# Kernel tuning notes

Hardware: AMD Instinct MI355X
Metric: run time of the kernel (lower is better)

Reference implementation:

```python
import jax, jax.numpy as jnp
import numpy as np
from jax import lax

GAMMA = 0.1  # fixed RBF bandwidth from LearnableRBFInfluence


def setup_inputs() -> dict:
    key = jax.random.key(0)
    k1, k2, k3, k4 = jax.random.split(key, 4)
    B, H, W = 2, 256, 256
    NUM_FILTERS, KS, NUM_BASIS = 48, 7, 31
    u_log = jax.random.normal(k1, (B, 1, H, W), jnp.float32)
    f_log = jax.random.normal(k2, (B, 1, H, W), jnp.float32)
    filters = jax.random.normal(k3, (NUM_FILTERS, 1, KS, KS), jnp.float32) * 0.05
    rbf_weights = jax.random.normal(k4, (NUM_FILTERS, NUM_BASIS), jnp.float32) * 0.05
    lambda_param = jnp.float32(0.1)
    return {"u_log": u_log, "f_log": f_log, "filters": filters,
            "rbf_weights": rbf_weights, "lambda_param": lambda_param}


def reference(u_log, f_log, filters, rbf_weights, lambda_param):
    # Batched form of the per-filter loop:
    #   conv[i] = conv2d(u, k_i)  ->  one grouped conv with 48 output channels
    num_basis = rbf_weights.shape[1]
    mu = jnp.linspace(-1.0, 1.0, num_basis).astype(u_log.dtype)  # [K]

    dn = lax.conv_dimension_numbers(u_log.shape, filters.shape, ('NCHW', 'OIHW', 'NCHW'))
    conv = lax.conv_general_dilated(u_log, filters, (1, 1), 'SAME',
                                    dimension_numbers=dn)  # [B,48,H,W]

    # RBF influence, per filter channel c: phi = sum_k w[c,k] * exp(-(conv-mu_k)^2/(2 g^2))
    diff = conv[..., None] - mu                              # [B,48,H,W,K]
    rbf = jnp.exp(-(diff * diff) / (2.0 * GAMMA * GAMMA))
    phi = jnp.einsum('bchwk,ck->bchw', rbf, rbf_weights)     # [B,48,H,W]

    # Per-filter conv2d(phi_i, flip(k_i)) summed over i == single conv
    # with OIHW weight [1,48,7,7] built from spatially-flipped filters.
    kT = jnp.flip(filters, axis=(2, 3)).transpose(1, 0, 2, 3)  # [1,48,7,7]
    dn2 = lax.conv_dimension_numbers(phi.shape, kT.shape, ('NCHW', 'OIHW', 'NCHW'))
    diffusion = lax.conv_general_dilated(phi, kT, (1, 1), 'SAME',
                                         dimension_numbers=dn2)  # [B,1,H,W]

    reaction = lambda_param * (u_log - f_log)
    return u_log - diffusion - reaction
```

## Files before the change

kernel.cpp:

```cpp
#include <hip/hip_runtime.h>

#define HH 256
#define WW 256
#define NPIX (2 * HH * WW)
#define NC 48
#define NB 31
#define TP 192

#define OTY 32
#define OTX 64
#define PTY 38
#define PSTR2 76
#define N1ITEM 684

#define PADW 272
#define PADN (2 * PADW * PADW)

#define PW1N (24 * 49)
#define PW2N (48 * 8 * 7)

#define OT 32
#define PT 38
#define PSTR 44
#define UT 44
#define USTR 52


typedef float f32x2 __attribute__((ext_vector_type(2)));

__device__ __forceinline__ f32x2 splat2(float v) {
    f32x2 r; r.x = v; r.y = v; return r;
}
__device__ __forceinline__ f32x2 pkfma(f32x2 a, f32x2 b, f32x2 c) {
    return __builtin_elementwise_fma(a, b, c);
}

__global__ __launch_bounds__(256)
void tnrd_prep(const float* __restrict__ wr,
               const float* __restrict__ u,
               const float* __restrict__ wf,
               float2* __restrict__ tab,
               float* __restrict__ upad,
               float2* __restrict__ pw1,
               float2* __restrict__ pw2)
{
    const int bid = blockIdx.x;
    const int tid = threadIdx.x;
    {
        const int i = bid * 256 + tid;
        const int img = i / (PADW * PADW);
        const int rem = i - img * (PADW * PADW);
        const int py = rem / PADW, px = rem - py * PADW;
        const int gy = py - 6, gx = px - 6;
        float v = 0.f;
        if ((unsigned)gy < HH && (unsigned)gx < WW)
            v = u[img * (HH * WW) + gy * WW + gx];
        upad[i] = v;
    }
    if (bid < NC && tid < TP) {
        const int j = tid;
        const float* rc = wr + bid * NB;
        float v0 = 0.f, v1 = 0.f;
        float x0 = fmaf((float)j, 1.0f / 64.0f, -1.5f);
        float x1 = x0 + 1.0f / 64.0f;
        #pragma unroll
        for (int k = 0; k < NB; ++k) {
            float mu = -1.f + (float)k * (1.f / 15.f);
            float d0 = x0 - mu, d1 = x1 - mu;
            float w = rc[k];
            v0 = fmaf(w, __expf(-50.f * d0 * d0), v0);
            v1 = fmaf(w, __expf(-50.f * d1 * d1), v1);
        }
        tab[bid * TP + j] = make_float2(v0, v1 - v0);
    }
    if (bid == 48) {
        for (int i = tid; i < PW1N; i += 256) {
            int pr = i / 49, k = i - pr * 49;
            pw1[i] = make_float2(wf[(2 * pr) * 49 + k],
                                 wf[(2 * pr + 1) * 49 + k]);
        }
    }
    if (bid == 49) {
        for (int i = tid; i < PW2N; i += 256) {
            int c = i / 56, r = i - c * 56;
            int dyt = r / 7, wi = r - dyt * 7;
            float lo = (dyt < 7) ? wf[c * 49 + (6 - dyt) * 7 + wi] : 0.f;
            float hi = (dyt > 0) ? wf[c * 49 + (7 - dyt) * 7 + wi] : 0.f;
            pw2[i] = make_float2(lo, hi);
        }
    }
}

__global__ __launch_bounds__(256)
void tnrd_table(const float* __restrict__ wr, float2* __restrict__ tab)
{
    const int ch = blockIdx.x;
    const float* rc = wr + ch * NB;
    for (int j = threadIdx.x; j < TP; j += 256) {
        float v0 = 0.f, v1 = 0.f;
        float x0 = fmaf((float)j, 1.0f / 64.0f, -1.5f);
        float x1 = x0 + 1.0f / 64.0f;
        #pragma unroll
        for (int k = 0; k < NB; ++k) {
            float mu = -1.f + (float)k * (1.f / 15.f);
            float d0 = x0 - mu, d1 = x1 - mu;
            float w = rc[k];
            v0 = fmaf(w, __expf(-50.f * d0 * d0), v0);
            v1 = fmaf(w, __expf(-50.f * d1 * d1), v1);
        }
        tab[ch * TP + j] = make_float2(v0, v1 - v0);
    }
}

#define F1STEPP(WI, s0, s1, s2, s3)                                     \
    { f32x2 w_ = wp[WI];                                                \
      ab0 = pkfma(splat2(s0), w_, ab0);                                 \
      ab1 = pkfma(splat2(s1), w_, ab1);                                 \
      ab2 = pkfma(splat2(s2), w_, ab2);                                 \
      ab3 = pkfma(splat2(s3), w_, ab3); }

#define F1ROWP(WPROW, q0, q1, q2)                                       \
    { const f32x2* wp = (WPROW);                                        \
      F1STEPP(0, q0.x, q0.y, q0.z, q0.w)                                \
      F1STEPP(1, q0.y, q0.z, q0.w, q1.x)                                \
      F1STEPP(2, q0.z, q0.w, q1.x, q1.y)                                \
      F1STEPP(3, q0.w, q1.x, q1.y, q1.z)                                \
      F1STEPP(4, q1.x, q1.y, q1.z, q1.w)                                \
      F1STEPP(5, q1.y, q1.z, q1.w, q2.x)                                \
      F1STEPP(6, q1.z, q1.w, q2.x, q2.y) }

#define LERP1(res, aval, T)                                             \
    { float t_ = fminf(fmaxf(fmaf(aval, 64.f, 96.f), 0.f), 191.999f);   \
      float fj_ = floorf(t_);                                           \
      float2 e_ = (T)[(int)fj_];               \
      res = fmaf(t_ - fj_, e_.y, e_.x); }

#define C2STEPP(WI, s0, s1, s2, s3, t0, t1, t2, t3)                     \
    { f32x2 wa_ = wpa[WI], wb_ = wpb[WI];                               \
      oo0 = pkfma(splat2(s0), wa_, oo0);                                \
      oo1 = pkfma(splat2(s1), wa_, oo1);                                \
      oo2 = pkfma(splat2(s2), wa_, oo2);                                \
      oo3 = pkfma(splat2(s3), wa_, oo3);                                \
      oo0 = pkfma(splat2(t0), wb_, oo0);                                \
      oo1 = pkfma(splat2(t1), wb_, oo1);                                \
      oo2 = pkfma(splat2(t2), wb_, oo2);                                \
      oo3 = pkfma(splat2(t3), wb_, oo3); }

#define C2SWEEPP()                                                      \
    C2STEPP(6, A0.x, A0.y, A0.z, A0.w, B0.x, B0.y, B0.z, B0.w)          \
    C2STEPP(5, A0.y, A0.z, A0.w, A1.x, B0.y, B0.z, B0.w, B1.x)          \
    C2STEPP(4, A0.z, A0.w, A1.x, A1.y, B0.z, B0.w, B1.x, B1.y)          \
    C2STEPP(3, A0.w, A1.x, A1.y, A1.z, B0.w, B1.x, B1.y, B1.z)          \
    C2STEPP(2, A1.x, A1.y, A1.z, A1.w, B1.x, B1.y, B1.z, B1.w)          \
    C2STEPP(1, A1.y, A1.z, A1.w, A2.x, B1.y, B1.z, B1.w, B2.x)          \
    C2STEPP(0, A1.z, A1.w, A2.x, A2.y, B1.z, B1.w, B2.x, B2.y)

__global__ __launch_bounds__(256, 6)
void tnrd_main_pk(const float* __restrict__ upad,
                  const f32x2* __restrict__ pw1,
                  const f32x2* __restrict__ pw2,
                  const float2* __restrict__ tab,
                  float* __restrict__ part)
{
    __shared__ __align__(16) float phi_s[2][PTY * PSTR2];

    const int tid = threadIdx.x;
    const int bx = blockIdx.x, by = blockIdx.y;
    const int b = blockIdx.z / 24, g = blockIdx.z % 24;
    const int c0 = g * 2;

    const int py0 = by * OTY - 3, px0 = bx * OTX - 3;

    {
        const f32x2* wpb0 = pw1 + g * 49;
        const float2* tA = tab + c0 * TP;
        const float2* tB = tA + TP;
        const float* ubase = upad + b * (PADW * PADW);
        for (int p = 0; p < 3; ++p) {
            const int gi = tid + p * 256;
            if (gi < N1ITEM) {
                const int pr = gi / 18, pc = (gi % 18) * 4;
                f32x2 ab0 = {0.f, 0.f}, ab1 = {0.f, 0.f};
                f32x2 ab2 = {0.f, 0.f}, ab3 = {0.f, 0.f};
                const float* bptr = ubase + (py0 + pr + 3) * PADW
                                          + (bx * OTX + pc);

                float4 c0v = *(const float4*)(bptr);
                float4 c1v = *(const float4*)(bptr + 4);
                float2 c2v = *(const float2*)(bptr + 8);
                #pragma unroll 1
                for (int dy = 0; dy < 6; ++dy) {
                    const float* nr = bptr + (dy + 1) * PADW;
                    float4 n0 = *(const float4*)(nr);
                    float4 n1 = *(const float4*)(nr + 4);
                    float2 n2 = *(const float2*)(nr + 8);
                    F1ROWP(wpb0 + dy * 7, c0v, c1v, c2v)
                    c0v = n0; c1v = n1; c2v = n2;
                }
                F1ROWP(wpb0 + 42, c0v, c1v, c2v)

                const int gy = py0 + pr;
                const bool rowok = (unsigned)gy < HH;
                const bool ok0 = rowok && (unsigned)(px0 + pc + 0) < WW;
                const bool ok1 = rowok && (unsigned)(px0 + pc + 1) < WW;
                const bool ok2 = rowok && (unsigned)(px0 + pc + 2) < WW;
                const bool ok3 = rowok && (unsigned)(px0 + pc + 3) < WW;
                float pA0, pA1, pA2, pA3, pB0, pB1, pB2, pB3;
                LERP1(pA0, ab0.x, tA) LERP1(pB0, ab0.y, tB)
                LERP1(pA1, ab1.x, tA) LERP1(pB1, ab1.y, tB)
                LERP1(pA2, ab2.x, tA) LERP1(pB2, ab2.y, tB)
                LERP1(pA3, ab3.x, tA) LERP1(pB3, ab3.y, tB)
                pA0 = ok0 ? pA0 : 0.f;  pB0 = ok0 ? pB0 : 0.f;
                pA1 = ok1 ? pA1 : 0.f;  pB1 = ok1 ? pB1 : 0.f;
                pA2 = ok2 ? pA2 : 0.f;  pB2 = ok2 ? pB2 : 0.f;
                pA3 = ok3 ? pA3 : 0.f;  pB3 = ok3 ? pB3 : 0.f;
                *(float4*)(&phi_s[0][pr * PSTR2 + pc]) =
                    make_float4(pA0, pA1, pA2, pA3);
                *(float4*)(&phi_s[1][pr * PSTR2 + pc]) =
                    make_float4(pB0, pB1, pB2, pB3);
            }
        }
    }
    __syncthreads();

    {
        const int tr = tid >> 4;
        const int ox = (tid & 15) * 4;
        f32x2 oo0 = {0.f, 0.f}, oo1 = {0.f, 0.f};
        f32x2 oo2 = {0.f, 0.f}, oo3 = {0.f, 0.f};

        #pragma unroll
        for (int dyt = 0; dyt < 8; ++dyt) {
            const float* rA = &phi_s[0][(2 * tr + dyt) * PSTR2 + ox];
            const float* rB = &phi_s[1][(2 * tr + dyt) * PSTR2 + ox];
            const float4 A0 = *(const float4*)(rA);
            const float4 A1 = *(const float4*)(rA + 4);
            const float2 A2 = *(const float2*)(rA + 8);
            const float4 B0 = *(const float4*)(rB);
            const float4 B1 = *(const float4*)(rB + 4);
            const float2 B2 = *(const float2*)(rB + 8);
            const f32x2* wpa = pw2 + (size_t)c0 * 56 + dyt * 7;
            const f32x2* wpb = wpa + 56;
            C2SWEEPP()
        }

        const int gy0 = by * OTY + 2 * tr, gx = bx * OTX + ox;
        float* dst = part + (size_t)g * NPIX + b * (HH * WW) + gy0 * WW + gx;
        *reinterpret_cast<float4*>(dst) =
            make_float4(oo0.x, oo1.x, oo2.x, oo3.x);
        *reinterpret_cast<float4*>(dst + WW) =
            make_float4(oo0.y, oo1.y, oo2.y, oo3.y);
    }
}

#define F1STEP(WI, s0, s1, s2, s3)                                      \
    { float fa = wa[WI], fb = wb[WI];                                   \
      a0 = fmaf(s0, fa, a0); a1 = fmaf(s1, fa, a1);                     \
      a2 = fmaf(s2, fa, a2); a3 = fmaf(s3, fa, a3);                     \
      b0 = fmaf(s0, fb, b0); b1 = fmaf(s1, fb, b1);                     \
      b2 = fmaf(s2, fb, b2); b3 = fmaf(s3, fb, b3); }

#define F1ROW(WA, WB, q0, q1, q2)                                       \
    { const float* wa = (WA); const float* wb = (WB);                   \
      F1STEP(0, q0.x, q0.y, q0.z, q0.w)                                 \
      F1STEP(1, q0.y, q0.z, q0.w, q1.x)                                 \
      F1STEP(2, q0.z, q0.w, q1.x, q1.y)                                 \
      F1STEP(3, q0.w, q1.x, q1.y, q1.z)                                 \
      F1STEP(4, q1.x, q1.y, q1.z, q1.w)                                 \
      F1STEP(5, q1.y, q1.z, q1.w, q2.x)                                 \
      F1STEP(6, q1.z, q1.w, q2.x, q2.y) }

#define C2STEP(WI, s0, s1, s2, s3, t0, t1, t2, t3)                      \
    { float fa = wra[WI], fb = wrb[WI];                                 \
      o0 = fmaf(s0, fa, o0); o1 = fmaf(s1, fa, o1);                     \
      o2 = fmaf(s2, fa, o2); o3 = fmaf(s3, fa, o3);                     \
      o0 = fmaf(t0, fb, o0); o1 = fmaf(t1, fb, o1);                     \
      o2 = fmaf(t2, fb, o2); o3 = fmaf(t3, fb, o3); }

template<int CPG>
__global__ __launch_bounds__(256, 6)
void tnrd_main(const float* __restrict__ u,
               const float* __restrict__ wf,
               const float2* __restrict__ tab,
               float* __restrict__ part)
{
    constexpr int NGRP = NC / CPG;
    constexpr int NPASS = CPG / 2;
    __shared__ __align__(16) float u_s[UT * USTR];
    __shared__ __align__(16) float phi_s[2][PT * PSTR];

    const int tid = threadIdx.x;
    const int bx = blockIdx.x, by = blockIdx.y;
    const int b = blockIdx.z / NGRP, g = blockIdx.z % NGRP;
    const int c0g = g * CPG;

    const int uy0 = by * OT - 6, ux0 = bx * OT - 6;
    const float* ub = u + b * (HH * WW);
    for (int i = tid; i < UT * USTR; i += 256) {
        int r = i / USTR, c = i - r * USTR;
        int gy = uy0 + r, gx = ux0 + c;
        float v = 0.f;
        if (c < UT && (unsigned)gy < HH && (unsigned)gx < WW)
            v = ub[gy * WW + gx];
        u_s[i] = v;
    }
    __syncthreads();

    const int oy = tid >> 3;
    const int ox0 = (tid & 7) * 4;
    float o0 = 0.f, o1 = 0.f, o2 = 0.f, o3 = 0.f;
    const int py0 = by * OT - 3, px0 = bx * OT - 3;

    auto conv1_pass = [&](int cp, float* __restrict__ bufA,
                          float* __restrict__ bufB) {
        const float* wA = wf + (c0g + 2 * cp) * 49;
        const float* wB = wA + 49;
        const float2* tA = tab + (c0g + 2 * cp) * TP;
        const float2* tB = tA + TP;
        for (int p = 0; p < 2; ++p) {
            const int gi = tid + p * 256;
            if (gi < PT * 10) {
                const int pr = gi % PT, pc = (gi / PT) * 4;
                float a0 = 0.f, a1 = 0.f, a2 = 0.f, a3 = 0.f;
                float b0 = 0.f, b1 = 0.f, b2 = 0.f, b3 = 0.f;
                const float* bptr = &u_s[pr * USTR + pc];
                float4 c0 = *(const float4*)(bptr);
                float4 c1 = *(const float4*)(bptr + 4);
                float2 c2 = *(const float2*)(bptr + 8);
                #pragma unroll 1
                for (int dy = 0; dy < 6; ++dy) {
                    const float* nr = bptr + (dy + 1) * USTR;
                    float4 n0 = *(const float4*)(nr);
                    float4 n1 = *(const float4*)(nr + 4);
                    float2 n2 = *(const float2*)(nr + 8);
                    F1ROW(wA + dy * 7, wB + dy * 7, c0, c1, c2)
                    c0 = n0; c1 = n1; c2 = n2;
                }
                F1ROW(wA + 42, wB + 42, c0, c1, c2)
                const int gy = py0 + pr;
                const bool rowok = (unsigned)gy < HH;
                const bool ok0 = rowok && (unsigned)(px0 + pc + 0) < WW;
                const bool ok1 = rowok && (unsigned)(px0 + pc + 1) < WW;
                const bool ok2 = rowok && (unsigned)(px0 + pc + 2) < WW;
                const bool ok3 = rowok && (unsigned)(px0 + pc + 3) < WW;
                float pA0, pA1, pA2, pA3, pB0, pB1, pB2, pB3;
                LERP1(pA0, a0, tA) LERP1(pB0, b0, tB)
                LERP1(pA1, a1, tA) LERP1(pB1, b1, tB)
                LERP1(pA2, a2, tA) LERP1(pB2, b2, tB)
                LERP1(pA3, a3, tA) LERP1(pB3, b3, tB)
                pA0 = ok0 ? pA0 : 0.f;  pB0 = ok0 ? pB0 : 0.f;
                pA1 = ok1 ? pA1 : 0.f;  pB1 = ok1 ? pB1 : 0.f;
                pA2 = ok2 ? pA2 : 0.f;  pB2 = ok2 ? pB2 : 0.f;
                pA3 = ok3 ? pA3 : 0.f;  pB3 = ok3 ? pB3 : 0.f;
                *(float4*)(bufA + pr * PSTR + pc) =
                    make_float4(pA0, pA1, pA2, pA3);
                *(float4*)(bufB + pr * PSTR + pc) =
                    make_float4(pB0, pB1, pB2, pB3);
            }
        }
    };

    #pragma unroll 1
    for (int pass = 0; pass < NPASS; ++pass) {
        conv1_pass(pass, phi_s[0], phi_s[1]);
        __syncthreads();
        const float* wA = wf + (c0g + 2 * pass) * 49;
        const float* wB = wA + 49;
        const float* pA = phi_s[0];
        const float* pB = phi_s[1];
        for (int dy = 0; dy < 7; ++dy) {
            const float* rA = pA + (oy + dy) * PSTR + ox0;
            const float* rB = pB + (oy + dy) * PSTR + ox0;
            const float4 A0 = *(const float4*)(rA);
            const float4 A1 = *(const float4*)(rA + 4);
            const float2 A2 = *(const float2*)(rA + 8);
            const float4 B0 = *(const float4*)(rB);
            const float4 B1 = *(const float4*)(rB + 4);
            const float2 B2 = *(const float2*)(rB + 8);
            const float* wra = wA + (6 - dy) * 7;
            const float* wrb = wB + (6 - dy) * 7;
            C2STEP(6, A0.x, A0.y, A0.z, A0.w, B0.x, B0.y, B0.z, B0.w)
            C2STEP(5, A0.y, A0.z, A0.w, A1.x, B0.y, B0.z, B0.w, B1.x)
            C2STEP(4, A0.z, A0.w, A1.x, A1.y, B0.z, B0.w, B1.x, B1.y)
            C2STEP(3, A0.w, A1.x, A1.y, A1.z, B0.w, B1.x, B1.y, B1.z)
            C2STEP(2, A1.x, A1.y, A1.z, A1.w, B1.x, B1.y, B1.z, B1.w)
            C2STEP(1, A1.y, A1.z, A1.w, A2.x, B1.y, B1.z, B1.w, B2.x)
            C2STEP(0, A1.z, A1.w, A2.x, A2.y, B1.z, B1.w, B2.x, B2.y)
        }
        if (pass < NPASS - 1) __syncthreads();
    }

    const int gy = by * OT + oy, gx = bx * OT + ox0;
    float4 v4 = make_float4(o0, o1, o2, o3);
    *reinterpret_cast<float4*>(part + (size_t)g * NPIX + b * (HH * WW)
                               + gy * WW + gx) = v4;
}

template<int NGRP>
__global__ __launch_bounds__(256)
void combine_kernel(const float* __restrict__ u,
                    const float* __restrict__ f,
                    const float* __restrict__ lam,
                    const float* __restrict__ part,
                    float* __restrict__ out)
{
    int i = blockIdx.x * 256 + threadIdx.x;
    float d = 0.f;
    #pragma unroll
    for (int g = 0; g < NGRP; ++g) d += part[g * NPIX + i];
    float lv = lam[0];
    float uv = u[i];
    float fv = f[i];
    out[i] = uv - d - lv * (uv - fv);
}

extern "C" void kernel_launch(void* const* d_in, const int* in_sizes, int n_in,
                              void* d_out, int out_size, void* d_ws, size_t ws_size,
                              hipStream_t stream) {
    const float* u    = (const float*)d_in[0];
    const float* f    = (const float*)d_in[1];
    const float* filt = (const float*)d_in[2];
    const float* rbfw = (const float*)d_in[3];
    const float* lam  = (const float*)d_in[4];
    float* out = (float*)d_out;
    float* part = (float*)d_ws;
    float2* tabg = (float2*)d_out;

    float* upad = part + (size_t)24 * NPIX;
    float* pw1f = upad + PADN;
    float* pw2f = pw1f + 2 * PW1N;
    const size_t need =
        ((size_t)24 * NPIX + PADN + 2 * PW1N + 2 * PW2N) * sizeof(float);
    if (ws_size >= need) {
        tnrd_prep<<<PADN / 256, 256, 0, stream>>>(
            rbfw, u, filt, tabg, upad, (float2*)pw1f, (float2*)pw2f);
        tnrd_main_pk<<<dim3(WW / OTX, HH / OTY, 48), 256, 0, stream>>>(
            upad, (const f32x2*)pw1f, (const f32x2*)pw2f, tabg, part);
        combine_kernel<24><<<512, 256, 0, stream>>>(u, f, lam, part, out);
    } else if (ws_size >= (size_t)12 * NPIX * sizeof(float)) {
        tnrd_table<<<NC, 256, 0, stream>>>(rbfw, tabg);
        tnrd_main<4><<<dim3(8, 8, 24), 256, 0, stream>>>(u, filt, tabg, part);
        combine_kernel<12><<<512, 256, 0, stream>>>(u, f, lam, part, out);
    } else {
        tnrd_table<<<NC, 256, 0, stream>>>(rbfw, tabg);
        tnrd_main<8><<<dim3(8, 8, 12), 256, 0, stream>>>(u, filt, tabg, part);
        combine_kernel<6><<<512, 256, 0, stream>>>(u, f, lam, part, out);
    }
}
```

Baseline: 95.83 us.

## Stage RBF tables in LDS and software-pipeline both conv stages

Each block now copies its two channels' RBF lookup tables into shared memory, so the per-pixel table gathers hit LDS instead of global memory. The first conv stage is unrolled into explicit work items whose table gathers are issued before earlier items are finished, letting gather latency overlap the next item's FMA work. The second conv stage double-buffers its LDS row loads so the next row is fetched while the current one is being used. In exchange the kernel needs more registers and an extra barrier, which may lower occupancy under the 6-blocks-per-SM launch bound.

```diff
diff --git a/kernel.cpp b/kernel.cpp
--- a/kernel.cpp
+++ b/kernel.cpp
@@ -129,11 +129,68 @@
       F1STEPP(5, q1.y, q1.z, q1.w, q2.x)                                \
       F1STEPP(6, q1.z, q1.w, q2.x, q2.y) }
 
-#define LERP1(res, aval, T)                                             \
+#define GISS(fr, e, aval, T)                                            \
     { float t_ = fminf(fmaxf(fmaf(aval, 64.f, 96.f), 0.f), 191.999f);   \
       float fj_ = floorf(t_);                                           \
-      float2 e_ = (T)[(int)fj_];               \
-      res = fmaf(t_ - fj_, e_.y, e_.x); }
+      fr = t_ - fj_;                                                    \
+      e = (T)[(int)fj_]; }
+
+#define C1_CONV(S, GI)                                                  \
+    const int pr##S = (GI) / 18, pc##S = ((GI) % 18) * 4;               \
+    f32x2 aba##S = {0.f, 0.f}, abb##S = {0.f, 0.f},                     \
+          abc##S = {0.f, 0.f}, abd##S = {0.f, 0.f};                     \
+    {                                                                   \
+        f32x2 &ab0 = aba##S, &ab1 = abb##S, &ab2 = abc##S, &ab3 = abd##S;\
+        const float* bptr = ubase + (py0 + pr##S + 3) * PADW            \
+                                  + (bx * OTX + pc##S);                 \
+        float4 c0v = *(const float4*)(bptr);                            \
+        float4 c1v = *(const float4*)(bptr + 4);                        \
+        float2 c2v = *(const float2*)(bptr + 8);                        \
+        _Pragma("unroll 1")                                             \
+        for (int dy = 0; dy < 6; ++dy) {                                \
+            const float* nr = bptr + (dy + 1) * PADW;                   \
+            float4 n0 = *(const float4*)(nr);                           \
+            float4 n1 = *(const float4*)(nr + 4);                       \
+            float2 n2 = *(const float2*)(nr + 8);                       \
+            F1ROWP(wpb0 + dy * 7, c0v, c1v, c2v)                        \
+            c0v = n0; c1v = n1; c2v = n2;                               \
+        }                                                               \
+        F1ROWP(wpb0 + 42, c0v, c1v, c2v)                                \
+    }
+
+#define C1_GATHER(S)                                                    \
+    float fA0##S, fA1##S, fA2##S, fA3##S, fB0##S, fB1##S, fB2##S, fB3##S;\
+    float2 eA0##S, eA1##S, eA2##S, eA3##S, eB0##S, eB1##S, eB2##S, eB3##S;\
+    GISS(fA0##S, eA0##S, aba##S.x, tAl) GISS(fB0##S, eB0##S, aba##S.y, tBl)\
+    GISS(fA1##S, eA1##S, abb##S.x, tAl) GISS(fB1##S, eB1##S, abb##S.y, tBl)\
+    GISS(fA2##S, eA2##S, abc##S.x, tAl) GISS(fB2##S, eB2##S, abc##S.y, tBl)\
+    GISS(fA3##S, eA3##S, abd##S.x, tAl) GISS(fB3##S, eB3##S, abd##S.y, tBl)
+
+#define C1_FIN(S)                                                       \
+    {                                                                   \
+        const int gy = py0 + pr##S;                                     \
+        const bool rowok = (unsigned)gy < HH;                           \
+        const bool ok0 = rowok && (unsigned)(px0 + pc##S + 0) < WW;     \
+        const bool ok1 = rowok && (unsigned)(px0 + pc##S + 1) < WW;     \
+        const bool ok2 = rowok && (unsigned)(px0 + pc##S + 2) < WW;     \
+        const bool ok3 = rowok && (unsigned)(px0 + pc##S + 3) < WW;     \
+        float pA0 = fmaf(fA0##S, eA0##S.y, eA0##S.x);                   \
+        float pB0 = fmaf(fB0##S, eB0##S.y, eB0##S.x);                   \
+        float pA1 = fmaf(fA1##S, eA1##S.y, eA1##S.x);                   \
+        float pB1 = fmaf(fB1##S, eB1##S.y, eB1##S.x);                   \
+        float pA2 = fmaf(fA2##S, eA2##S.y, eA2##S.x);                   \
+        float pB2 = fmaf(fB2##S, eB2##S.y, eB2##S.x);                   \
+        float pA3 = fmaf(fA3##S, eA3##S.y, eA3##S.x);                   \
+        float pB3 = fmaf(fB3##S, eB3##S.y, eB3##S.x);                   \
+        pA0 = ok0 ? pA0 : 0.f;  pB0 = ok0 ? pB0 : 0.f;                  \
+        pA1 = ok1 ? pA1 : 0.f;  pB1 = ok1 ? pB1 : 0.f;                  \
+        pA2 = ok2 ? pA2 : 0.f;  pB2 = ok2 ? pB2 : 0.f;                  \
+        pA3 = ok3 ? pA3 : 0.f;  pB3 = ok3 ? pB3 : 0.f;                  \
+        *(float4*)(&phi_s[0][pr##S * PSTR2 + pc##S]) =                  \
+            make_float4(pA0, pA1, pA2, pA3);                            \
+        *(float4*)(&phi_s[1][pr##S * PSTR2 + pc##S]) =                  \
+            make_float4(pB0, pB1, pB2, pB3);                            \
+    }
 
 #define C2STEPP(WI, s0, s1, s2, s3, t0, t1, t2, t3)                     \
     { f32x2 wa_ = wpa[WI], wb_ = wpb[WI];                               \
@@ -156,69 +213,43 @@
     C2STEPP(0, A1.z, A1.w, A2.x, A2.y, B1.z, B1.w, B2.x, B2.y)
 
 __global__ __launch_bounds__(256, 6)
-void tnrd_main_pk(const float* __restrict__ upad,
+void tnrd_main_pl(const float* __restrict__ upad,
                   const f32x2* __restrict__ pw1,
                   const f32x2* __restrict__ pw2,
                   const float2* __restrict__ tab,
                   float* __restrict__ part)
 {
     __shared__ __align__(16) float phi_s[2][PTY * PSTR2];
+    __shared__ __align__(16) float2 tabs[2][TP];
 
     const int tid = threadIdx.x;
     const int bx = blockIdx.x, by = blockIdx.y;
     const int b = blockIdx.z / 24, g = blockIdx.z % 24;
     const int c0 = g * 2;
 
+    for (int i = tid; i < 2 * TP; i += 256)
+        ((float2*)tabs)[i] = tab[c0 * TP + i];
+    __syncthreads();
+
     const int py0 = by * OTY - 3, px0 = bx * OTX - 3;
+    const f32x2* wpb0 = pw1 + g * 49;
+    const float2* tAl = tabs[0];
+    const float2* tBl = tabs[1];
+    const float* ubase = upad + b * (PADW * PADW);
 
     {
-        const f32x2* wpb0 = pw1 + g * 49;
-        const float2* tA = tab + c0 * TP;
-        const float2* tB = tA + TP;
-        const float* ubase = upad + b * (PADW * PADW);
-        for (int p = 0; p < 3; ++p) {
-            const int gi = tid + p * 256;
-            if (gi < N1ITEM) {
-                const int pr = gi / 18, pc = (gi % 18) * 4;
-                f32x2 ab0 = {0.f, 0.f}, ab1 = {0.f, 0.f};
-                f32x2 ab2 = {0.f, 0.f}, ab3 = {0.f, 0.f};
-                const float* bptr = ubase + (py0 + pr + 3) * PADW
-                                          + (bx * OTX + pc);
-
-                float4 c0v = *(const float4*)(bptr);
-                float4 c1v = *(const float4*)(bptr + 4);
-                float2 c2v = *(const float2*)(bptr + 8);
-                #pragma unroll 1
-                for (int dy = 0; dy < 6; ++dy) {
-                    const float* nr = bptr + (dy + 1) * PADW;
-                    float4 n0 = *(const float4*)(nr);
-                    float4 n1 = *(const float4*)(nr + 4);
-                    float2 n2 = *(const float2*)(nr + 8);
-                    F1ROWP(wpb0 + dy * 7, c0v, c1v, c2v)
-                    c0v = n0; c1v = n1; c2v = n2;
-                }
-                F1ROWP(wpb0 + 42, c0v, c1v, c2v)
-
-                const int gy = py0 + pr;
-                const bool rowok = (unsigned)gy < HH;
-                const bool ok0 = rowok && (unsigned)(px0 + pc + 0) < WW;
-                const bool ok1 = rowok && (unsigned)(px0 + pc + 1) < WW;
-                const bool ok2 = rowok && (unsigned)(px0 + pc + 2) < WW;
-                const bool ok3 = rowok && (unsigned)(px0 + pc + 3) < WW;
-                float pA0, pA1, pA2, pA3, pB0, pB1, pB2, pB3;
-                LERP1(pA0, ab0.x, tA) LERP1(pB0, ab0.y, tB)
-                LERP1(pA1, ab1.x, tA) LERP1(pB1, ab1.y, tB)
-                LERP1(pA2, ab2.x, tA) LERP1(pB2, ab2.y, tB)
-                LERP1(pA3, ab3.x, tA) LERP1(pB3, ab3.y, tB)
-                pA0 = ok0 ? pA0 : 0.f;  pB0 = ok0 ? pB0 : 0.f;
-                pA1 = ok1 ? pA1 : 0.f;  pB1 = ok1 ? pB1 : 0.f;
-                pA2 = ok2 ? pA2 : 0.f;  pB2 = ok2 ? pB2 : 0.f;
-                pA3 = ok3 ? pA3 : 0.f;  pB3 = ok3 ? pB3 : 0.f;
-                *(float4*)(&phi_s[0][pr * PSTR2 + pc]) =
-                    make_float4(pA0, pA1, pA2, pA3);
-                *(float4*)(&phi_s[1][pr * PSTR2 + pc]) =
-                    make_float4(pB0, pB1, pB2, pB3);
-            }
+        C1_CONV(X, tid)
+        C1_GATHER(X)
+        C1_CONV(Y, tid + 256)
+        C1_GATHER(Y)
+        C1_FIN(X)
+        if (tid < N1ITEM - 512) {
+            C1_CONV(Z, tid + 512)
+            C1_GATHER(Z)
+            C1_FIN(Y)
+            C1_FIN(Z)
+        } else {
+            C1_FIN(Y)
         }
     }
     __syncthreads();
@@ -229,19 +260,39 @@
         f32x2 oo0 = {0.f, 0.f}, oo1 = {0.f, 0.f};
         f32x2 oo2 = {0.f, 0.f}, oo3 = {0.f, 0.f};
 
+        const float* rA0 = &phi_s[0][(2 * tr) * PSTR2 + ox];
+        const float* rB0 = &phi_s[1][(2 * tr) * PSTR2 + ox];
+        float4 A0c = *(const float4*)(rA0);
+        float4 A1c = *(const float4*)(rA0 + 4);
+        float2 A2c = *(const float2*)(rA0 + 8);
+        float4 B0c = *(const float4*)(rB0);
+        float4 B1c = *(const float4*)(rB0 + 4);
+        float2 B2c = *(const float2*)(rB0 + 8);
+
         #pragma unroll
         for (int dyt = 0; dyt < 8; ++dyt) {
-            const float* rA = &phi_s[0][(2 * tr + dyt) * PSTR2 + ox];
-            const float* rB = &phi_s[1][(2 * tr + dyt) * PSTR2 + ox];
-            const float4 A0 = *(const float4*)(rA);
-            const float4 A1 = *(const float4*)(rA + 4);
-            const float2 A2 = *(const float2*)(rA + 8);
-            const float4 B0 = *(const float4*)(rB);
-            const float4 B1 = *(const float4*)(rB + 4);
-            const float2 B2 = *(const float2*)(rB + 8);
-            const f32x2* wpa = pw2 + (size_t)c0 * 56 + dyt * 7;
-            const f32x2* wpb = wpa + 56;
-            C2SWEEPP()
+            float4 A0n, A1n, B0n, B1n; float2 A2n, B2n;
+            if (dyt < 7) {
+                const float* nA = &phi_s[0][(2 * tr + dyt + 1) * PSTR2 + ox];
+                const float* nB = &phi_s[1][(2 * tr + dyt + 1) * PSTR2 + ox];
+                A0n = *(const float4*)(nA);
+                A1n = *(const float4*)(nA + 4);
+                A2n = *(const float2*)(nA + 8);
+                B0n = *(const float4*)(nB);
+                B1n = *(const float4*)(nB + 4);
+                B2n = *(const float2*)(nB + 8);
+            }
+            {
+                const float4 A0 = A0c, A1 = A1c; const float2 A2 = A2c;
+                const float4 B0 = B0c, B1 = B1c; const float2 B2 = B2c;
+                const f32x2* wpa = pw2 + (size_t)c0 * 56 + dyt * 7;
+                const f32x2* wpb = wpa + 56;
+                C2SWEEPP()
+            }
+            if (dyt < 7) {
+                A0c = A0n; A1c = A1n; A2c = A2n;
+                B0c = B0n; B1c = B1n; B2c = B2n;
+            }
         }
 
         const int gy0 = by * OTY + 2 * tr, gx = bx * OTX + ox;
@@ -269,6 +320,12 @@
       F1STEP(4, q1.x, q1.y, q1.z, q1.w)                                 \
       F1STEP(5, q1.y, q1.z, q1.w, q2.x)                                 \
       F1STEP(6, q1.z, q1.w, q2.x, q2.y) }
+
+#define LERP1(res, aval, T)                                             \
+    { float t_ = fminf(fmaxf(fmaf(aval, 64.f, 96.f), 0.f), 191.999f);   \
+      float fj_ = floorf(t_);                                           \
+      float2 e_ = (T)[(int)fj_];                                        \
+      res = fmaf(t_ - fj_, e_.y, e_.x); }
 
 #define C2STEP(WI, s0, s1, s2, s3, t0, t1, t2, t3)                      \
     { float fa = wra[WI], fb = wrb[WI];                                 \
@@ -434,7 +491,7 @@
     if (ws_size >= need) {
         tnrd_prep<<<PADN / 256, 256, 0, stream>>>(
             rbfw, u, filt, tabg, upad, (float2*)pw1f, (float2*)pw2f);
-        tnrd_main_pk<<<dim3(WW / OTX, HH / OTY, 48), 256, 0, stream>>>(
+        tnrd_main_pl<<<dim3(WW / OTX, HH / OTY, 48), 256, 0, stream>>>(
             upad, (const f32x2*)pw1f, (const f32x2*)pw2f, tabg, part);
         combine_kernel<24><<<512, 256, 0, stream>>>(u, f, lam, part, out);
     } else if (ws_size >= (size_t)12 * NPIX * sizeof(float)) {
```

Result: no change. 95.35 us, median of 2 (-0.5%).

## Split fused conv kernel into separate phi and diffusion kernels via global phi buffer

Applied to the files above, without the earlier changes.

The single fused kernel, which recomputed a halo of phi in shared memory for each output tile, is split into two kernels. tnrd_conv1 writes phi for all 48 channels into padded global planes without recomputing the halo, and tnrd_conv2 reads those planes to do the second 7x7 convolution. The prep kernel now zeroes the border of the phi planes. This removes the redundant halo computation and the __syncthreads, but adds about 28 MB of extra global traffic and another kernel launch.

```diff
diff --git a/kernel.cpp b/kernel.cpp
--- a/kernel.cpp
+++ b/kernel.cpp
@@ -7,14 +7,14 @@
 #define NB 31
 #define TP 192
 
-#define OTY 32
-#define OTX 64
-#define PTY 38
-#define PSTR2 76
-#define N1ITEM 684
-
 #define PADW 272
 #define PADN (2 * PADW * PADW)
+
+#define PPW 272
+#define PPSZ (PPW * PPW)
+#define NPLANE (NC * 2)
+#define ZPP 3936
+#define ZTOT (NPLANE * ZPP)
 
 #define PW1N (24 * 49)
 #define PW2N (48 * 8 * 7)
@@ -41,21 +41,38 @@
                const float* __restrict__ wf,
                float2* __restrict__ tab,
                float* __restrict__ upad,
+               float* __restrict__ phig,
                float2* __restrict__ pw1,
                float2* __restrict__ pw2)
 {
     const int bid = blockIdx.x;
     const int tid = threadIdx.x;
+    const int gtid = bid * 256 + tid;
     {
-        const int i = bid * 256 + tid;
+        const int i = gtid;
         const int img = i / (PADW * PADW);
         const int rem = i - img * (PADW * PADW);
         const int py = rem / PADW, px = rem - py * PADW;
-        const int gy = py - 6, gx = px - 6;
+        const int gy = py - 7, gx = px - 7;
         float v = 0.f;
         if ((unsigned)gy < HH && (unsigned)gx < WW)
             v = u[img * (HH * WW) + gy * WW + gx];
         upad[i] = v;
+    }
+    for (int i = gtid; i < ZTOT; i += PADN) {
+        const int pl = i / ZPP, idx = i - pl * ZPP;
+        int row, col;
+        if (idx < 6 * PPW) {
+            const int r = idx / PPW;
+            row = (r < 3) ? 4 + r : 260 + r;
+            col = idx - r * PPW;
+        } else {
+            const int j = idx - 6 * PPW;
+            const int c9 = j % 9;
+            col = (c9 < 3) ? 4 + c9 : 260 + c9;
+            row = 7 + j / 9;
+        }
+        phig[(size_t)pl * PPSZ + row * PPW + col] = 0.f;
     }
     if (bid < NC && tid < TP) {
         const int j = tid;
@@ -132,7 +149,7 @@
 #define LERP1(res, aval, T)                                             \
     { float t_ = fminf(fmaxf(fmaf(aval, 64.f, 96.f), 0.f), 191.999f);   \
       float fj_ = floorf(t_);                                           \
-      float2 e_ = (T)[(int)fj_];               \
+      float2 e_ = (T)[(int)fj_];                                        \
       res = fmaf(t_ - fj_, e_.y, e_.x); }
 
 #define C2STEPP(WI, s0, s1, s2, s3, t0, t1, t2, t3)                     \
@@ -155,102 +172,99 @@
     C2STEPP(1, A1.y, A1.z, A1.w, A2.x, B1.y, B1.z, B1.w, B2.x)          \
     C2STEPP(0, A1.z, A1.w, A2.x, A2.y, B1.z, B1.w, B2.x, B2.y)
 
-__global__ __launch_bounds__(256, 6)
-void tnrd_main_pk(const float* __restrict__ upad,
-                  const f32x2* __restrict__ pw1,
-                  const f32x2* __restrict__ pw2,
-                  const float2* __restrict__ tab,
-                  float* __restrict__ part)
-{
-    __shared__ __align__(16) float phi_s[2][PTY * PSTR2];
-
+__global__ __launch_bounds__(256, 7)
+void tnrd_conv1(const float* __restrict__ upad,
+                const f32x2* __restrict__ pw1,
+                const float2* __restrict__ tab,
+                float* __restrict__ phig)
+{
     const int tid = threadIdx.x;
     const int bx = blockIdx.x, by = blockIdx.y;
     const int b = blockIdx.z / 24, g = blockIdx.z % 24;
     const int c0 = g * 2;
 
-    const int py0 = by * OTY - 3, px0 = bx * OTX - 3;
-
-    {
-        const f32x2* wpb0 = pw1 + g * 49;
-        const float2* tA = tab + c0 * TP;
-        const float2* tB = tA + TP;
-        const float* ubase = upad + b * (PADW * PADW);
-        for (int p = 0; p < 3; ++p) {
-            const int gi = tid + p * 256;
-            if (gi < N1ITEM) {
-                const int pr = gi / 18, pc = (gi % 18) * 4;
-                f32x2 ab0 = {0.f, 0.f}, ab1 = {0.f, 0.f};
-                f32x2 ab2 = {0.f, 0.f}, ab3 = {0.f, 0.f};
-                const float* bptr = ubase + (py0 + pr + 3) * PADW
-                                          + (bx * OTX + pc);
-
-                float4 c0v = *(const float4*)(bptr);
-                float4 c1v = *(const float4*)(bptr + 4);
-                float2 c2v = *(const float2*)(bptr + 8);
-                #pragma unroll 1
-                for (int dy = 0; dy < 6; ++dy) {
-                    const float* nr = bptr + (dy + 1) * PADW;
-                    float4 n0 = *(const float4*)(nr);
-                    float4 n1 = *(const float4*)(nr + 4);
-                    float2 n2 = *(const float2*)(nr + 8);
-                    F1ROWP(wpb0 + dy * 7, c0v, c1v, c2v)
-                    c0v = n0; c1v = n1; c2v = n2;
-                }
-                F1ROWP(wpb0 + 42, c0v, c1v, c2v)
-
-                const int gy = py0 + pr;
-                const bool rowok = (unsigned)gy < HH;
-                const bool ok0 = rowok && (unsigned)(px0 + pc + 0) < WW;
-                const bool ok1 = rowok && (unsigned)(px0 + pc + 1) < WW;
-                const bool ok2 = rowok && (unsigned)(px0 + pc + 2) < WW;
-                const bool ok3 = rowok && (unsigned)(px0 + pc + 3) < WW;
-                float pA0, pA1, pA2, pA3, pB0, pB1, pB2, pB3;
-                LERP1(pA0, ab0.x, tA) LERP1(pB0, ab0.y, tB)
-                LERP1(pA1, ab1.x, tA) LERP1(pB1, ab1.y, tB)
-                LERP1(pA2, ab2.x, tA) LERP1(pB2, ab2.y, tB)
-                LERP1(pA3, ab3.x, tA) LERP1(pB3, ab3.y, tB)
-                pA0 = ok0 ? pA0 : 0.f;  pB0 = ok0 ? pB0 : 0.f;
-                pA1 = ok1 ? pA1 : 0.f;  pB1 = ok1 ? pB1 : 0.f;
-                pA2 = ok2 ? pA2 : 0.f;  pB2 = ok2 ? pB2 : 0.f;
-                pA3 = ok3 ? pA3 : 0.f;  pB3 = ok3 ? pB3 : 0.f;
-                *(float4*)(&phi_s[0][pr * PSTR2 + pc]) =
-                    make_float4(pA0, pA1, pA2, pA3);
-                *(float4*)(&phi_s[1][pr * PSTR2 + pc]) =
-                    make_float4(pB0, pB1, pB2, pB3);
-            }
-        }
-    }
-    __syncthreads();
-
-    {
-        const int tr = tid >> 4;
-        const int ox = (tid & 15) * 4;
-        f32x2 oo0 = {0.f, 0.f}, oo1 = {0.f, 0.f};
-        f32x2 oo2 = {0.f, 0.f}, oo3 = {0.f, 0.f};
-
-        #pragma unroll
-        for (int dyt = 0; dyt < 8; ++dyt) {
-            const float* rA = &phi_s[0][(2 * tr + dyt) * PSTR2 + ox];
-            const float* rB = &phi_s[1][(2 * tr + dyt) * PSTR2 + ox];
-            const float4 A0 = *(const float4*)(rA);
-            const float4 A1 = *(const float4*)(rA + 4);
-            const float2 A2 = *(const float2*)(rA + 8);
-            const float4 B0 = *(const float4*)(rB);
-            const float4 B1 = *(const float4*)(rB + 4);
-            const float2 B2 = *(const float2*)(rB + 8);
-            const f32x2* wpa = pw2 + (size_t)c0 * 56 + dyt * 7;
-            const f32x2* wpb = wpa + 56;
-            C2SWEEPP()
-        }
-
-        const int gy0 = by * OTY + 2 * tr, gx = bx * OTX + ox;
-        float* dst = part + (size_t)g * NPIX + b * (HH * WW) + gy0 * WW + gx;
-        *reinterpret_cast<float4*>(dst) =
-            make_float4(oo0.x, oo1.x, oo2.x, oo3.x);
-        *reinterpret_cast<float4*>(dst + WW) =
-            make_float4(oo0.y, oo1.y, oo2.y, oo3.y);
-    }
+    const int gy0 = by * 32, gx0 = bx * 32;
+    const int pr = tid >> 3;
+    const int pc = (tid & 7) * 4;
+
+    const f32x2* wpb0 = pw1 + g * 49;
+    const float2* tA = tab + c0 * TP;
+    const float2* tB = tA + TP;
+    const float* ubase = upad + b * (PADW * PADW);
+
+    f32x2 ab0 = {0.f, 0.f}, ab1 = {0.f, 0.f};
+    f32x2 ab2 = {0.f, 0.f}, ab3 = {0.f, 0.f};
+    const float* bptr = ubase + (gy0 + pr + 4) * PADW + (gx0 + pc + 4);
+
+    float4 c0v = *(const float4*)(bptr);
+    float4 c1v = *(const float4*)(bptr + 4);
+    float2 c2v = *(const float2*)(bptr + 8);
+    #pragma unroll 1
+    for (int dy = 0; dy < 6; ++dy) {
+        const float* nr = bptr + (dy + 1) * PADW;
+        float4 n0 = *(const float4*)(nr);
+        float4 n1 = *(const float4*)(nr + 4);
+        float2 n2 = *(const float2*)(nr + 8);
+        F1ROWP(wpb0 + dy * 7, c0v, c1v, c2v)
+        c0v = n0; c1v = n1; c2v = n2;
+    }
+    F1ROWP(wpb0 + 42, c0v, c1v, c2v)
+
+    float pA0, pA1, pA2, pA3, pB0, pB1, pB2, pB3;
+    LERP1(pA0, ab0.x, tA) LERP1(pB0, ab0.y, tB)
+    LERP1(pA1, ab1.x, tA) LERP1(pB1, ab1.y, tB)
+    LERP1(pA2, ab2.x, tA) LERP1(pB2, ab2.y, tB)
+    LERP1(pA3, ab3.x, tA) LERP1(pB3, ab3.y, tB)
+
+    float* dA = phig + (size_t)(c0 * 2 + b) * PPSZ
+              + (7 + gy0 + pr) * PPW + (7 + gx0 + pc);
+    float* dB = dA + 2 * PPSZ;
+    dA[0] = pA0; dA[1] = pA1; dA[2] = pA2; dA[3] = pA3;
+    dB[0] = pB0; dB[1] = pB1; dB[2] = pB2; dB[3] = pB3;
+}
+
+__global__ __launch_bounds__(256, 8)
+void tnrd_conv2(const float* __restrict__ phig,
+                const f32x2* __restrict__ pw2,
+                float* __restrict__ part)
+{
+    const int tid = threadIdx.x;
+    const int bx = blockIdx.x, by = blockIdx.y;
+    const int b = blockIdx.z / 24, g = blockIdx.z % 24;
+    const int c0 = g * 2;
+
+    const int gy0 = by * 32, gx0 = bx * 64;
+    const int tr = tid >> 4;
+    const int ox = (tid & 15) * 4;
+
+    const float* pA = phig + (size_t)(c0 * 2 + b) * PPSZ;
+    const float* pB = pA + 2 * PPSZ;
+
+    f32x2 oo0 = {0.f, 0.f}, oo1 = {0.f, 0.f};
+    f32x2 oo2 = {0.f, 0.f}, oo3 = {0.f, 0.f};
+
+    #pragma unroll
+    for (int dyt = 0; dyt < 8; ++dyt) {
+        const int row = gy0 + 2 * tr + dyt + 4;
+        const float* rA = pA + row * PPW + (gx0 + ox + 4);
+        const float* rB = pB + row * PPW + (gx0 + ox + 4);
+        const float4 A0 = *(const float4*)(rA);
+        const float4 A1 = *(const float4*)(rA + 4);
+        const float2 A2 = *(const float2*)(rA + 8);
+        const float4 B0 = *(const float4*)(rB);
+        const float4 B1 = *(const float4*)(rB + 4);
+        const float2 B2 = *(const float2*)(rB + 8);
+        const f32x2* wpa = pw2 + (size_t)c0 * 56 + dyt * 7;
+        const f32x2* wpb = wpa + 56;
+        C2SWEEPP()
+    }
+
+    const int gyo = gy0 + 2 * tr, gx = gx0 + ox;
+    float* dst = part + (size_t)g * NPIX + b * (HH * WW) + gyo * WW + gx;
+    *reinterpret_cast<float4*>(dst) =
+        make_float4(oo0.x, oo1.x, oo2.x, oo3.x);
+    *reinterpret_cast<float4*>(dst + WW) =
+        make_float4(oo0.y, oo1.y, oo2.y, oo3.y);
 }
 
 #define F1STEP(WI, s0, s1, s2, s3)                                      \
@@ -429,13 +443,16 @@
     float* upad = part + (size_t)24 * NPIX;
     float* pw1f = upad + PADN;
     float* pw2f = pw1f + 2 * PW1N;
-    const size_t need =
-        ((size_t)24 * NPIX + PADN + 2 * PW1N + 2 * PW2N) * sizeof(float);
+    float* phig = pw2f + 2 * PW2N;
+    const size_t need = ((size_t)24 * NPIX + PADN + 2 * PW1N + 2 * PW2N
+                         + (size_t)NPLANE * PPSZ) * sizeof(float);
     if (ws_size >= need) {
         tnrd_prep<<<PADN / 256, 256, 0, stream>>>(
-            rbfw, u, filt, tabg, upad, (float2*)pw1f, (float2*)pw2f);
-        tnrd_main_pk<<<dim3(WW / OTX, HH / OTY, 48), 256, 0, stream>>>(
-            upad, (const f32x2*)pw1f, (const f32x2*)pw2f, tabg, part);
+            rbfw, u, filt, tabg, upad, phig, (float2*)pw1f, (float2*)pw2f);
+        tnrd_conv1<<<dim3(8, 8, 48), 256, 0, stream>>>(
+            upad, (const f32x2*)pw1f, tabg, phig);
+        tnrd_conv2<<<dim3(4, 8, 48), 256, 0, stream>>>(
+            phig, (const f32x2*)pw2f, part);
         combine_kernel<24><<<512, 256, 0, stream>>>(u, f, lam, part, out);
     } else if (ws_size >= (size_t)12 * NPIX * sizeof(float)) {
         tnrd_table<<<NC, 256, 0, stream>>>(rbfw, tabg);
```

Measured after the change: 108.0 us. 12.7% more time.
